# Optimization experiments

Measured on AMD Instinct MI355X. Metric: run time of the kernel, lower is better.

## Reference

```python
import jax, jax.numpy as jnp
import numpy as np

N_NODES = 50000
N_EDGES = 1600000
D_IN = 48
D_OUT = 48


def setup_inputs() -> dict:
    key = jax.random.key(0)
    k1, k2, k3, k4 = jax.random.split(key, 4)
    features = jax.random.normal(k1, (N_NODES, D_IN), dtype=jnp.float32)
    src = jax.random.randint(k2, (N_EDGES,), 0, N_NODES, dtype=jnp.int64)
    dst = jax.random.randint(k3, (N_EDGES,), 0, N_NODES, dtype=jnp.int64)
    # xavier_normal for Linear(48,48): std = sqrt(2/(fan_in+fan_out))
    std = np.sqrt(2.0 / (D_IN + D_OUT))
    W = jax.random.normal(k4, (D_OUT, D_IN), dtype=jnp.float32) * std
    b = jnp.zeros((D_OUT,), dtype=jnp.float32)
    return {"features": features, "src": src, "dst": dst, "W": W, "b": b}


def reference(features, src, dst, W, b):
    n = features.shape[0]
    ones = jnp.ones(src.shape[0], dtype=features.dtype)
    out_deg = jax.ops.segment_sum(ones, src, num_segments=n)
    in_deg = jax.ops.segment_sum(ones, dst, num_segments=n)
    ci = jax.lax.rsqrt(jnp.maximum(out_deg, 1.0))  # per src node
    cj = jax.lax.rsqrt(jnp.maximum(in_deg, 1.0))   # per dst node
    # gather-scale: m_e = h[src_e] * ci[src_e]
    msg = features[src] * ci[src][:, None]          # [E, D_IN]
    # scatter-sum to dst, then scale by cj
    agg = jax.ops.segment_sum(msg, dst, num_segments=n) * cj[:, None]
    # DGL update_all leaves zero-in-degree nodes with their original 'h'
    h = jnp.where(in_deg[:, None] > 0, agg, features)
    out = jax.nn.relu(h @ W.T + b)
    return out
```

## Files before the change

kernel.cpp:

```cpp
#include <hip/hip_runtime.h>
#include <hip/hip_fp16.h>

#define N_NODES 50000
#define N_EDGES 1600000
#define D 48

#define EPB 8192
#define PB  196
#define NPB_D 50
#define NBIN_D 1000
#define NPB_S 256
#define NBIN_S 196

#define EMAX 2400
#define HS 52

#define RECD_OFF  0
#define SRCB_OFF  6422528
#define OFFLD_OFF 8028160
#define OFFLS_OFF 8420552
#define CI_OFF    8497776
#define SFEAT_OFF 8697776
#define SFEAT_END 13497776

__global__ __launch_bounds__(1024) void k_prep(const int* __restrict__ src,
                                               const int* __restrict__ dst,
                                               unsigned int* __restrict__ rec,
                                               unsigned char* __restrict__ srcb,
                                               unsigned short* __restrict__ offld,
                                               unsigned short* __restrict__ offls) {
    __shared__ int cd[NBIN_D];
    __shared__ int cs[NBIN_S];
    __shared__ int wsum[16], wexcl[16];
    __shared__ int wsum2[4], wexcl2[4];
    __shared__ alignas(16) unsigned int  bufd[EPB];
    __shared__ alignas(16) unsigned char bufs[EPB];
    int tid = threadIdx.x, p = blockIdx.x;
    int wave = tid >> 6, lane = tid & 63;
    int base = p * EPB;

    int sv[8], dv[8];
    bool ok[8];
    #pragma unroll
    for (int k = 0; k < 8; ++k) {
        int e = base + tid + k * 1024;
        ok[k] = (e < N_EDGES);
        sv[k] = ok[k] ? src[e] : 0;
        dv[k] = ok[k] ? dst[e] : 0;
    }

    for (int i = tid; i < NBIN_D; i += 1024) cd[i] = 0;
    for (int i = tid; i < NBIN_S; i += 1024) cs[i] = 0;
    __syncthreads();
    #pragma unroll
    for (int k = 0; k < 8; ++k) {
        if (ok[k]) {
            atomicAdd(&cd[dv[k] / NPB_D], 1);
            atomicAdd(&cs[sv[k] >> 8], 1);
        }
    }
    __syncthreads();

    int own = (tid < NBIN_D) ? cd[tid] : 0;
    int incl = own;
    #pragma unroll
    for (int o = 1; o < 64; o <<= 1) {
        int u = __shfl_up(incl, o);
        if (lane >= o) incl += u;
    }
    if (lane == 63) wsum[wave] = incl;
    __syncthreads();
    if (tid < 16) {
        int v = wsum[tid];
        int ic = v;
        #pragma unroll
        for (int o = 1; o < 16; o <<= 1) {
            int u = __shfl_up(ic, o);
            if (lane >= o) ic += u;
        }
        wexcl[tid] = ic - v;
    }
    __syncthreads();
    if (tid < NBIN_D) {
        int gincl = wexcl[wave] + incl;
        int ex = gincl - own;
        offld[p * (NBIN_D + 1) + tid] = (unsigned short)ex;
        cd[tid] = ex;
        if (tid == NBIN_D - 1) offld[p * (NBIN_D + 1) + NBIN_D] = (unsigned short)gincl;
    }

    int own2 = (tid < NBIN_S) ? cs[tid] : 0;
    int incl2 = own2;
    #pragma unroll
    for (int o = 1; o < 64; o <<= 1) {
        int u = __shfl_up(incl2, o);
        if (lane >= o) incl2 += u;
    }
    if (lane == 63 && wave < 4) wsum2[wave] = incl2;
    __syncthreads();
    if (tid < 4) {
        int v = wsum2[tid];
        int ic = v;
        #pragma unroll
        for (int o = 1; o < 4; o <<= 1) {
            int u = __shfl_up(ic, o);
            if (lane >= o) ic += u;
        }
        wexcl2[tid] = ic - v;
    }
    __syncthreads();
    if (tid < NBIN_S) {
        int gincl2 = wexcl2[wave] + incl2;
        int ex = gincl2 - own2;
        offls[p * (NBIN_S + 1) + tid] = (unsigned short)ex;
        cs[tid] = ex;
        if (tid == NBIN_S - 1) offls[p * (NBIN_S + 1) + NBIN_S] = (unsigned short)gincl2;
    }
    __syncthreads();

    #pragma unroll
    for (int k = 0; k < 8; ++k) {
        if (ok[k]) {
            int s = sv[k], d = dv[k];
            int bin = d / NPB_D;
            int pd = atomicAdd(&cd[bin], 1);
            bufd[pd] = ((unsigned int)s << 6) | (unsigned int)(d - bin * NPB_D);
            int ps = atomicAdd(&cs[s >> 8], 1);
            bufs[ps] = (unsigned char)s;
        }
    }
    __syncthreads();

    int4* ro = (int4*)(rec + base);
    const int4* bi = (const int4*)bufd;
    for (int i = tid; i < EPB / 4; i += 1024) ro[i] = bi[i];
    unsigned int* so = (unsigned int*)(srcb + base);
    const unsigned int* bs = (const unsigned int*)bufs;
    for (int i = tid; i < EPB / 4; i += 1024) so[i] = bs[i];
}

__global__ __launch_bounds__(512) void k_ci(const unsigned char* __restrict__ srcb,
                                            const unsigned short* __restrict__ offls,
                                            const float* __restrict__ feat,
                                            float* __restrict__ ci,
                                            __half* __restrict__ sfeat,
                                            int do_scale) {
    __shared__ int cnt[NPB_S];
    __shared__ float cl[NPB_S];
    int tid = threadIdx.x, sb = blockIdx.x;
    for (int i = tid; i < NPB_S; i += 512) cnt[i] = 0;
    __syncthreads();
    int wave = tid >> 6, lane = tid & 63;
    for (int p = wave; p < PB; p += 8) {
        int beg = offls[p * (NBIN_S + 1) + sb];
        int end = offls[p * (NBIN_S + 1) + sb + 1];
        for (int j = beg + lane; j < end; j += 64)
            atomicAdd(&cnt[srcb[p * EPB + j]], 1);
    }
    __syncthreads();
    if (tid < NPB_S) {
        float c = rsqrtf(fmaxf((float)cnt[tid], 1.0f));
        cl[tid] = c;
        int n = sb * NPB_S + tid;
        if (n < N_NODES) ci[n] = c;
    }
    __syncthreads();
    if (do_scale) {
        int nb = sb * NPB_S;
        int lim2 = (min(NPB_S, N_NODES - nb)) * 24;
        const float2* f2 = (const float2*)feat + (size_t)nb * 24;
        __half2* s2 = (__half2*)sfeat + (size_t)nb * 24;
        for (int i = tid; i < lim2; i += 512) {
            float sc = cl[i / 24];
            float2 f = f2[i];
            s2[i] = __float22half2_rn(make_float2(f.x * sc, f.y * sc));
        }
    }
}

template <bool PRESCALED>
__global__ __launch_bounds__(512, 8) void k_gcn(
    const unsigned int* __restrict__ rec, const unsigned short* __restrict__ offld,
    const float* __restrict__ ci, const __half* __restrict__ sfeat,
    const float* __restrict__ feat,
    const float* __restrict__ W, const float* __restrict__ b,
    float* __restrict__ out) {
    __shared__ int   colb[EMAX];
    __shared__ float hl[NPB_D * HS];
    __shared__ float Wl[D * HS];
    __shared__ float bl[D];
    __shared__ int   ideg[NPB_D];
    __shared__ int   off[NPB_D];
    __shared__ int   cur[NPB_D];
    __shared__ int   runoff[PB + 1];
    __shared__ int   runpos[PB];
    __shared__ int   wsum[8], wexcl[8];
    int tid = threadIdx.x, bin = blockIdx.x;
    int wave = tid >> 6, lane = tid & 63;

    for (int i = tid; i < D * D; i += 512) Wl[(i / D) * HS + (i % D)] = W[i];
    if (tid < D) bl[tid] = b[tid];
    if (tid < NPB_D) { ideg[tid] = 0; cur[tid] = 0; }

    int rlen = 0;
    if (tid < PB) {
        int o0 = offld[tid * (NBIN_D + 1) + bin];
        int o1 = offld[tid * (NBIN_D + 1) + bin + 1];
        rlen = o1 - o0;
        runpos[tid] = tid * EPB + o0;
    }
    int incl = rlen;
    #pragma unroll
    for (int o = 1; o < 64; o <<= 1) {
        int u = __shfl_up(incl, o);
        if (lane >= o) incl += u;
    }
    if (lane == 63) wsum[wave] = incl;
    __syncthreads();
    if (tid < 8) {
        int v = wsum[tid];
        int ic = v;
        #pragma unroll
        for (int o = 1; o < 8; o <<= 1) {
            int u = __shfl_up(ic, o);
            if (lane >= o) ic += u;
        }
        wexcl[tid] = ic - v;
        if (tid == 7) runoff[PB] = ic;
    }
    __syncthreads();
    if (tid < PB) runoff[tid] = wexcl[wave] + incl - rlen;
    __syncthreads();
    int cnt = runoff[PB];
    if (cnt > EMAX) cnt = EMAX;

    unsigned int rr[5];
    #pragma unroll
    for (int k = 0; k < 5; ++k) {
        int j = tid + k * 512;
        rr[k] = 0xFFFFFFFFu;
        if (j < cnt) {
            int lo = 0, hi = PB - 1;
            while (lo < hi) {
                int mid = (lo + hi + 1) >> 1;
                if (runoff[mid] <= j) lo = mid; else hi = mid - 1;
            }
            unsigned int r = rec[runpos[lo] + (j - runoff[lo])];
            rr[k] = r;
            atomicAdd(&ideg[r & 63], 1);
        }
    }
    __syncthreads();
    if (tid < NPB_D) {
        int v = ideg[tid];
        int ic = v;
        #pragma unroll
        for (int o = 1; o < 64; o <<= 1) {
            int u = __shfl_up(ic, o);
            if (tid >= o) ic += u;
        }
        off[tid] = ic - v;
    }
    __syncthreads();
    #pragma unroll
    for (int k = 0; k < 5; ++k) {
        if (rr[k] != 0xFFFFFFFFu) {
            int dl = rr[k] & 63;
            int p = atomicAdd(&cur[dl], 1);
            colb[off[dl] + p] = (int)(rr[k] >> 6);
        }
    }
    __syncthreads();

    int eslot = lane / 12;
    int d4 = lane - eslot * 12;
    bool lane_ok = (lane < 60);
    const float4* feat4 = (const float4*)feat;
    const uint2* sf = (const uint2*)sfeat;

    for (int q = 0; q < 7; ++q) {
        int nl = q * 8 + wave;
        if (nl >= NPB_D) break;
        int n = bin * NPB_D + nl;
        int cb = off[nl];
        int deg = ideg[nl];

        float4 acc = make_float4(0.0f, 0.0f, 0.0f, 0.0f);
        for (int i0 = 0; i0 < deg; i0 += 5) {
            int ei = i0 + eslot;
            bool act = lane_ok && (ei < deg);
            int s = act ? colb[cb + ei] : 0;
            if (act) {
                if (PRESCALED) {
                    uint2 u = sf[(size_t)s * 12 + d4];
                    __half2 ha = *reinterpret_cast<__half2*>(&u.x);
                    __half2 hb = *reinterpret_cast<__half2*>(&u.y);
                    float2 fa = __half22float2(ha);
                    float2 fb = __half22float2(hb);
                    acc.x += fa.x; acc.y += fa.y; acc.z += fb.x; acc.w += fb.y;
                } else {
                    float c = ci[s];
                    float4 f = feat4[(size_t)s * 12 + d4];
                    acc.x = fmaf(f.x, c, acc.x);
                    acc.y = fmaf(f.y, c, acc.y);
                    acc.z = fmaf(f.z, c, acc.z);
                    acc.w = fmaf(f.w, c, acc.w);
                }
            }
        }
        {
            float x1 = __shfl(acc.x, lane + 12), x2 = __shfl(acc.x, lane + 24);
            float x3 = __shfl(acc.x, lane + 36), x4 = __shfl(acc.x, lane + 48);
            float y1 = __shfl(acc.y, lane + 12), y2 = __shfl(acc.y, lane + 24);
            float y3 = __shfl(acc.y, lane + 36), y4 = __shfl(acc.y, lane + 48);
            float z1 = __shfl(acc.z, lane + 12), z2 = __shfl(acc.z, lane + 24);
            float z3 = __shfl(acc.z, lane + 36), z4 = __shfl(acc.z, lane + 48);
            float w1 = __shfl(acc.w, lane + 12), w2 = __shfl(acc.w, lane + 24);
            float w3 = __shfl(acc.w, lane + 36), w4 = __shfl(acc.w, lane + 48);
            acc.x += (x1 + x2) + (x3 + x4);
            acc.y += (y1 + y2) + (y3 + y4);
            acc.z += (z1 + z2) + (z3 + z4);
            acc.w += (w1 + w2) + (w3 + w4);
        }
        if (lane < 12) {
            float4 res;
            if (deg > 0) {
                float cj = rsqrtf((float)deg);
                res = make_float4(acc.x * cj, acc.y * cj, acc.z * cj, acc.w * cj);
            } else {
                res = feat4[(size_t)n * 12 + d4];
            }
            *(float4*)(hl + nl * HS + d4 * 4) = res;
        }
    }
    __syncthreads();

    #pragma unroll
    for (int half = 0; half < 2; ++half) {
        int nl = (tid >> 4) + half * 32;
        int c = tid & 15;
        if (nl < NPB_D) {
            int n = bin * NPB_D + nl;
            float a0 = bl[c], a1 = bl[c + 16], a2 = bl[c + 32];
            #pragma unroll
            for (int k4 = 0; k4 < 12; ++k4) {
                float4 hv = *(const float4*)(hl + nl * HS + k4 * 4);
                float4 w0 = *(const float4*)(Wl + c * HS + k4 * 4);
                float4 w1 = *(const float4*)(Wl + (c + 16) * HS + k4 * 4);
                float4 w2 = *(const float4*)(Wl + (c + 32) * HS + k4 * 4);
                a0 = fmaf(hv.x, w0.x, a0); a0 = fmaf(hv.y, w0.y, a0);
                a0 = fmaf(hv.z, w0.z, a0); a0 = fmaf(hv.w, w0.w, a0);
                a1 = fmaf(hv.x, w1.x, a1); a1 = fmaf(hv.y, w1.y, a1);
                a1 = fmaf(hv.z, w1.z, a1); a1 = fmaf(hv.w, w1.w, a1);
                a2 = fmaf(hv.x, w2.x, a2); a2 = fmaf(hv.y, w2.y, a2);
                a2 = fmaf(hv.z, w2.z, a2); a2 = fmaf(hv.w, w2.w, a2);
            }
            float* op = out + (size_t)n * D;
            op[c]      = fmaxf(a0, 0.0f);
            op[c + 16] = fmaxf(a1, 0.0f);
            op[c + 32] = fmaxf(a2, 0.0f);
        }
    }
}

extern "C" void kernel_launch(void* const* d_in, const int* in_sizes, int n_in,
                              void* d_out, int out_size, void* d_ws, size_t ws_size,
                              hipStream_t stream) {
    const float* feat = (const float*)d_in[0];
    const int*   src  = (const int*)d_in[1];
    const int*   dst  = (const int*)d_in[2];
    const float* W    = (const float*)d_in[3];
    const float* b    = (const float*)d_in[4];
    float* out = (float*)d_out;

    char* ws = (char*)d_ws;
    unsigned int*   rec   = (unsigned int*)(ws + RECD_OFF);
    unsigned char*  srcb  = (unsigned char*)(ws + SRCB_OFF);
    unsigned short* offld = (unsigned short*)(ws + OFFLD_OFF);
    unsigned short* offls = (unsigned short*)(ws + OFFLS_OFF);
    float*          ci    = (float*)(ws + CI_OFF);
    __half*         sfeat = (__half*)(ws + SFEAT_OFF);

    const bool prescale = (ws_size >= (size_t)SFEAT_END);

    k_prep<<<PB, 1024, 0, stream>>>(src, dst, rec, srcb, offld, offls);
    k_ci<<<NBIN_S, 512, 0, stream>>>(srcb, offls, feat, ci, sfeat, prescale ? 1 : 0);
    if (prescale)
        k_gcn<true><<<NBIN_D, 512, 0, stream>>>(rec, offld, ci, sfeat, feat, W, b, out);
    else
        k_gcn<false><<<NBIN_D, 512, 0, stream>>>(rec, offld, ci, sfeat, feat, W, b, out);
}
```

Baseline: 137.9 us.

## Widen gather loads to 16B per lane and use 8 edges per wave

The edge-index loads in the prep kernel now read src and dst as int4 vectors instead of scalars, which changes which edges each thread owns. The aggregation loop now gives each lane 8 fp16 features (a uint4) instead of 4, so a wave processes 8 edges per iteration rather than 5. It replaces the strided shuffle reduction with an xor butterfly. The aim is fewer, wider memory transactions for the random neighbour gather, at the cost of 2 idle lanes in every 8 (48 of 64 lanes active) and more registers per lane.

```diff
diff --git a/kernel.cpp b/kernel.cpp
--- a/kernel.cpp
+++ b/kernel.cpp
@@ -41,12 +41,19 @@
 
     int sv[8], dv[8];
     bool ok[8];
-    #pragma unroll
-    for (int k = 0; k < 8; ++k) {
-        int e = base + tid + k * 1024;
-        ok[k] = (e < N_EDGES);
-        sv[k] = ok[k] ? src[e] : 0;
-        dv[k] = ok[k] ? dst[e] : 0;
+    const int4* s4p = (const int4*)src;
+    const int4* d4p = (const int4*)dst;
+    #pragma unroll
+    for (int c = 0; c < 2; ++c) {
+        int e4 = base + c * 4096 + tid * 4;
+        bool v = (e4 < N_EDGES);
+        int4 s4 = v ? s4p[e4 >> 2] : make_int4(0, 0, 0, 0);
+        int4 d4 = v ? d4p[e4 >> 2] : make_int4(0, 0, 0, 0);
+        sv[c * 4 + 0] = s4.x; sv[c * 4 + 1] = s4.y;
+        sv[c * 4 + 2] = s4.z; sv[c * 4 + 3] = s4.w;
+        dv[c * 4 + 0] = d4.x; dv[c * 4 + 1] = d4.y;
+        dv[c * 4 + 2] = d4.z; dv[c * 4 + 3] = d4.w;
+        ok[c * 4 + 0] = v; ok[c * 4 + 1] = v; ok[c * 4 + 2] = v; ok[c * 4 + 3] = v;
     }
 
     for (int i = tid; i < NBIN_D; i += 1024) cd[i] = 0;
@@ -272,11 +279,11 @@
     }
     __syncthreads();
 
-    int eslot = lane / 12;
-    int d4 = lane - eslot * 12;
-    bool lane_ok = (lane < 60);
+    int eslot = lane >> 3;
+    int d8 = lane & 7;
+    bool lane_ok = (d8 < 6);
     const float4* feat4 = (const float4*)feat;
-    const uint2* sf = (const uint2*)sfeat;
+    const uint4* sf = (const uint4*)sfeat;
 
     for (int q = 0; q < 7; ++q) {
         int nl = q * 8 + wave;
@@ -285,52 +292,63 @@
         int cb = off[nl];
         int deg = ideg[nl];
 
-        float4 acc = make_float4(0.0f, 0.0f, 0.0f, 0.0f);
-        for (int i0 = 0; i0 < deg; i0 += 5) {
+        float4 accA = make_float4(0.0f, 0.0f, 0.0f, 0.0f);
+        float4 accB = make_float4(0.0f, 0.0f, 0.0f, 0.0f);
+        for (int i0 = 0; i0 < deg; i0 += 8) {
             int ei = i0 + eslot;
             bool act = lane_ok && (ei < deg);
             int s = act ? colb[cb + ei] : 0;
             if (act) {
                 if (PRESCALED) {
-                    uint2 u = sf[(size_t)s * 12 + d4];
-                    __half2 ha = *reinterpret_cast<__half2*>(&u.x);
-                    __half2 hb = *reinterpret_cast<__half2*>(&u.y);
-                    float2 fa = __half22float2(ha);
-                    float2 fb = __half22float2(hb);
-                    acc.x += fa.x; acc.y += fa.y; acc.z += fb.x; acc.w += fb.y;
+                    uint4 u = sf[(size_t)s * 6 + d8];
+                    __half2 h0 = *reinterpret_cast<__half2*>(&u.x);
+                    __half2 h1 = *reinterpret_cast<__half2*>(&u.y);
+                    __half2 h2 = *reinterpret_cast<__half2*>(&u.z);
+                    __half2 h3 = *reinterpret_cast<__half2*>(&u.w);
+                    float2 f0 = __half22float2(h0);
+                    float2 f1 = __half22float2(h1);
+                    float2 f2 = __half22float2(h2);
+                    float2 f3 = __half22float2(h3);
+                    accA.x += f0.x; accA.y += f0.y; accA.z += f1.x; accA.w += f1.y;
+                    accB.x += f2.x; accB.y += f2.y; accB.z += f3.x; accB.w += f3.y;
                 } else {
                     float c = ci[s];
-                    float4 f = feat4[(size_t)s * 12 + d4];
-                    acc.x = fmaf(f.x, c, acc.x);
-                    acc.y = fmaf(f.y, c, acc.y);
-                    acc.z = fmaf(f.z, c, acc.z);
-                    acc.w = fmaf(f.w, c, acc.w);
+                    float4 fa = feat4[(size_t)s * 12 + d8 * 2];
+                    float4 fb = feat4[(size_t)s * 12 + d8 * 2 + 1];
+                    accA.x = fmaf(fa.x, c, accA.x);
+                    accA.y = fmaf(fa.y, c, accA.y);
+                    accA.z = fmaf(fa.z, c, accA.z);
+                    accA.w = fmaf(fa.w, c, accA.w);
+                    accB.x = fmaf(fb.x, c, accB.x);
+                    accB.y = fmaf(fb.y, c, accB.y);
+                    accB.z = fmaf(fb.z, c, accB.z);
+                    accB.w = fmaf(fb.w, c, accB.w);
                 }
             }
         }
-        {
-            float x1 = __shfl(acc.x, lane + 12), x2 = __shfl(acc.x, lane + 24);
-            float x3 = __shfl(acc.x, lane + 36), x4 = __shfl(acc.x, lane + 48);
-            float y1 = __shfl(acc.y, lane + 12), y2 = __shfl(acc.y, lane + 24);
-            float y3 = __shfl(acc.y, lane + 36), y4 = __shfl(acc.y, lane + 48);
-            float z1 = __shfl(acc.z, lane + 12), z2 = __shfl(acc.z, lane + 24);
-            float z3 = __shfl(acc.z, lane + 36), z4 = __shfl(acc.z, lane + 48);
-            float w1 = __shfl(acc.w, lane + 12), w2 = __shfl(acc.w, lane + 24);
-            float w3 = __shfl(acc.w, lane + 36), w4 = __shfl(acc.w, lane + 48);
-            acc.x += (x1 + x2) + (x3 + x4);
-            acc.y += (y1 + y2) + (y3 + y4);
-            acc.z += (z1 + z2) + (z3 + z4);
-            acc.w += (w1 + w2) + (w3 + w4);
-        }
-        if (lane < 12) {
-            float4 res;
+        #pragma unroll
+        for (int m = 8; m <= 32; m <<= 1) {
+            accA.x += __shfl_xor(accA.x, m);
+            accA.y += __shfl_xor(accA.y, m);
+            accA.z += __shfl_xor(accA.z, m);
+            accA.w += __shfl_xor(accA.w, m);
+            accB.x += __shfl_xor(accB.x, m);
+            accB.y += __shfl_xor(accB.y, m);
+            accB.z += __shfl_xor(accB.z, m);
+            accB.w += __shfl_xor(accB.w, m);
+        }
+        if (lane < 6) {
+            float4 rA, rB;
             if (deg > 0) {
                 float cj = rsqrtf((float)deg);
-                res = make_float4(acc.x * cj, acc.y * cj, acc.z * cj, acc.w * cj);
+                rA = make_float4(accA.x * cj, accA.y * cj, accA.z * cj, accA.w * cj);
+                rB = make_float4(accB.x * cj, accB.y * cj, accB.z * cj, accB.w * cj);
             } else {
-                res = feat4[(size_t)n * 12 + d4];
+                rA = feat4[(size_t)n * 12 + lane * 2];
+                rB = feat4[(size_t)n * 12 + lane * 2 + 1];
             }
-            *(float4*)(hl + nl * HS + d4 * 4) = res;
+            *(float4*)(hl + nl * HS + lane * 8) = rA;
+            *(float4*)(hl + nl * HS + lane * 8 + 4) = rB;
         }
     }
     __syncthreads();
```

New measurement: 140.5 us. No clear change (+1.9%).
